# Kernel optimization log

Hardware: AMD Instinct MI355X
Metric: run time of the kernel (lower is better)

Reference implementation:

```python
import jax, jax.numpy as jnp
import numpy as np

D = 1024      # d_model
H = 16        # num_heads
DK = D // H   # head dim
L = 6         # num_layers
DFF = 4 * D   # feed-forward width
V = 32000     # vocab
B = 8         # batch
TP1 = 513     # target tokens (x length); decoded length = 512
S = 1024      # encoder frames
MAXLEN = 512
EPS = 1e-6


def make_pe(max_len, d):
    pos = np.arange(max_len, dtype=np.float64)[:, None]
    i = np.arange(0, d, 2, dtype=np.float64)[None, :]
    ang = pos / np.power(10000.0, i / d)
    pe = np.zeros((max_len, d), dtype=np.float32)
    pe[:, 0::2] = np.sin(ang)
    pe[:, 1::2] = np.cos(ang)
    return jnp.asarray(pe)


def setup_inputs() -> dict:
    key = jax.random.key(0)
    ks = jax.random.split(key, 16)
    sc = 0.02
    inp = {
        'x': jax.random.randint(ks[0], (B, TP1), 0, V, dtype=jnp.int64),
        'encoder_output': jax.random.normal(ks[1], (B, S, D), jnp.float32),
        'emb': jax.random.normal(ks[2], (V, D), jnp.float32) * sc,
        'pe': make_pe(MAXLEN, D),
        # per-layer stacked params; index 0..3 = q,k,v,out projections (in,out layout)
        'attn1_w': jax.random.normal(ks[3], (L, 4, D, D), jnp.float32) * sc,
        'attn1_b': jnp.zeros((L, 4, D), jnp.float32),
        'attn2_w': jax.random.normal(ks[4], (L, 4, D, D), jnp.float32) * sc,
        'attn2_b': jnp.zeros((L, 4, D), jnp.float32),
        'norm_a': jnp.ones((L, 3, D), jnp.float32),
        'norm_b': jnp.zeros((L, 3, D), jnp.float32),
        'ff1_w': jax.random.normal(ks[5], (L, D, DFF), jnp.float32) * sc,
        'ff1_b': jnp.zeros((L, DFF), jnp.float32),
        'ff2_w': jax.random.normal(ks[6], (L, DFF, D), jnp.float32) * sc,
        'ff2_b': jnp.zeros((L, D), jnp.float32),
        'fc_w': jax.random.normal(ks[7], (D, V), jnp.float32) * sc,
        'fc_b': jnp.zeros((V,), jnp.float32),
    }
    return inp


def _norm(x, a, b):
    mu = jnp.mean(x, axis=-1, keepdims=True)
    # torch .std() default is unbiased (ddof=1)
    var = jnp.sum((x - mu) ** 2, axis=-1, keepdims=True) / (x.shape[-1] - 1)
    return a * (x - mu) / (jnp.sqrt(var) + EPS) + b


def _mha(q_in, kv_in, w, b):
    # w: [4, D, D], b: [4, D]; masks in the original are no-ops (bug), omitted.
    bs, tq, _ = q_in.shape
    q = (q_in @ w[0] + b[0]).reshape(bs, tq, H, DK).transpose(0, 2, 1, 3)
    k = (kv_in @ w[1] + b[1]).reshape(bs, -1, H, DK).transpose(0, 2, 1, 3)
    v = (kv_in @ w[2] + b[2]).reshape(bs, -1, H, DK).transpose(0, 2, 1, 3)
    score = jnp.einsum('bhqd,bhkd->bhqk', q, k) / np.sqrt(DK).astype(np.float32)
    attn = jax.nn.softmax(score, axis=-1)
    o = jnp.einsum('bhqk,bhkd->bhqd', attn, v)
    o = o.transpose(0, 2, 1, 3).reshape(bs, tq, D)
    return o @ w[3] + b[3]


def reference(x, encoder_output, emb, pe, attn1_w, attn1_b, attn2_w, attn2_b,
              norm_a, norm_b, ff1_w, ff1_b, ff2_w, ff2_b, fc_w, fc_b):
    t = x.shape[1] - 1
    h = emb[x[:, :-1]] + pe[None, :t, :]  # [B, T, D]
    for l in range(L):
        a1 = _mha(h, h, attn1_w[l], attn1_b[l])
        h = _norm(a1 + h, norm_a[l, 0], norm_b[l, 0])
        a2 = _mha(h, encoder_output, attn2_w[l], attn2_b[l])
        h = _norm(a2 + h, norm_a[l, 1], norm_b[l, 1])
        f = jax.nn.relu(h @ ff1_w[l] + ff1_b[l]) @ ff2_w[l] + ff2_b[l]
        h = _norm(f + h, norm_a[l, 2], norm_b[l, 2])
    logits = h @ fc_w + fc_b  # [B, T, V]
    return jax.nn.log_softmax(logits, axis=-1)
```

## Files before the change

### kernel.cpp

```cpp
#include <hip/hip_runtime.h>

typedef __attribute__((ext_vector_type(4))) float f32x4;
typedef __attribute__((ext_vector_type(8))) __bf16 bfx8;
typedef unsigned short u16;
typedef unsigned int u32;

__device__ __forceinline__ u16 f2bf(float f) {
  u32 u = __builtin_bit_cast(u32, f);
  u = (u + 0x7FFFu + ((u >> 16) & 1u)) >> 16;
  return (u16)u;
}
__device__ __forceinline__ float bf2f(u16 u) {
  return __builtin_bit_cast(float, ((u32)u) << 16);
}

typedef __attribute__((address_space(1))) const void gvoid;
typedef __attribute__((address_space(3))) void svoid;
__device__ __forceinline__ void gload16(const void* g, void* l) {
  __builtin_amdgcn_global_load_lds((gvoid*)g, (svoid*)l, 16, 0, 0);
}

__device__ __forceinline__ float wredsum(float v) {
#pragma unroll
  for (int o = 32; o; o >>= 1) v += __shfl_xor(v, o, 64);
  return v;
}
__device__ __forceinline__ float wredmax(float v) {
#pragma unroll
  for (int o = 32; o; o >>= 1) v = fmaxf(v, __shfl_xor(v, o, 64));
  return v;
}

__global__ __launch_bounds__(256) void wconv_kernel(const float* __restrict__ in,
                                                    u16* __restrict__ out, int K, int N) {
  __shared__ u16 tile[32][33];
  const long z = blockIdx.z;
  const float* iz = in + z * (long)K * N;
  u16* oz = out + z * (long)K * N;
  const int n0 = blockIdx.x << 5, k0 = blockIdx.y << 5;
  const int tx = threadIdx.x & 31, ty = threadIdx.x >> 5;
#pragma unroll
  for (int i = 0; i < 4; ++i)
    tile[ty + 8 * i][tx] = f2bf(iz[(long)(k0 + ty + 8 * i) * N + n0 + tx]);
  __syncthreads();
#pragma unroll
  for (int i = 0; i < 4; ++i)
    oz[(long)(n0 + ty + 8 * i) * K + k0 + tx] = tile[tx][ty + 8 * i];
}

__global__ __launch_bounds__(256) void cvt_kernel(const float* __restrict__ in,
                                                  u16* __restrict__ out, long n) {
  long i = ((long)blockIdx.x * 256 + threadIdx.x) * 4;
  if (i + 3 < n) {
    float4 v = *(const float4*)(in + i);
    ushort4 o = {f2bf(v.x), f2bf(v.y), f2bf(v.z), f2bf(v.w)};
    *(ushort4*)(out + i) = o;
  }
}

__global__ __launch_bounds__(256) void embed_kernel(const int* __restrict__ x,
                                                    const float* __restrict__ emb,
                                                    const float* __restrict__ pe,
                                                    float* __restrict__ h,
                                                    u16* __restrict__ hb) {
  const int row = blockIdx.x;
  const int b = row >> 9, t = row & 511;
  const long tok = (long)x[b * 513 + t];
  const int d = threadIdx.x << 2;
  float4 e = *(const float4*)(emb + tok * 1024 + d);
  float4 p = *(const float4*)(pe + (long)t * 1024 + d);
  float4 v = {e.x + p.x, e.y + p.y, e.z + p.z, e.w + p.w};
  *(float4*)(h + (long)row * 1024 + d) = v;
  ushort4 o = {f2bf(v.x), f2bf(v.y), f2bf(v.z), f2bf(v.w)};
  *(ushort4*)(hb + (long)row * 1024 + d) = o;
}

__global__ __launch_bounds__(256) void addnorm_kernel(const float* __restrict__ delta,
                                                      const float* __restrict__ delta2,
                                                      float* __restrict__ h,
                                                      u16* __restrict__ hb,
                                                      const float* __restrict__ ga,
                                                      const float* __restrict__ gb) {
  __shared__ float r1[4], r2[4];
  const long row = blockIdx.x;
  const int d = threadIdx.x << 2;
  float4 a = *(const float4*)(h + row * 1024 + d);
  float4 q = *(const float4*)(delta + row * 1024 + d);
  float4 q2 = *(const float4*)(delta2 + row * 1024 + d);
  float x0 = a.x + q.x + q2.x, x1 = a.y + q.y + q2.y;
  float x2 = a.z + q.z + q2.z, x3 = a.w + q.w + q2.w;
  float s1 = wredsum(x0 + x1 + x2 + x3);
  float s2 = wredsum(x0 * x0 + x1 * x1 + x2 * x2 + x3 * x3);
  if ((threadIdx.x & 63) == 0) { r1[threadIdx.x >> 6] = s1; r2[threadIdx.x >> 6] = s2; }
  __syncthreads();
  float S1 = r1[0] + r1[1] + r1[2] + r1[3];
  float S2 = r2[0] + r2[1] + r2[2] + r2[3];
  float mu = S1 * (1.0f / 1024.0f);
  float var = (S2 - S1 * mu) * (1.0f / 1023.0f);
  float inv = 1.0f / (sqrtf(fmaxf(var, 0.f)) + 1e-6f);
  float4 g4 = *(const float4*)(ga + d);
  float4 b4 = *(const float4*)(gb + d);
  float y0 = g4.x * (x0 - mu) * inv + b4.x;
  float y1 = g4.y * (x1 - mu) * inv + b4.y;
  float y2 = g4.z * (x2 - mu) * inv + b4.z;
  float y3 = g4.w * (x3 - mu) * inv + b4.w;
  float4 y = {y0, y1, y2, y3};
  *(float4*)(h + row * 1024 + d) = y;
  ushort4 o = {f2bf(y0), f2bf(y1), f2bf(y2), f2bf(y3)};
  *(ushort4*)(hb + row * 1024 + d) = o;
}

__global__ __launch_bounds__(256) void logsoftmax_kernel(float* __restrict__ lg) {
  const long row = blockIdx.x;
  float* lr = lg + row * 32000L;
  float m = -1e30f, s = 0.f;
  for (int j = threadIdx.x; j < 8000; j += 256) {
    float4 v = *(const float4*)(lr + (long)j * 4);
    float lm = fmaxf(fmaxf(v.x, v.y), fmaxf(v.z, v.w));
    if (lm > m) { s *= __expf(m - lm); m = lm; }
    s += __expf(v.x - m) + __expf(v.y - m) + __expf(v.z - m) + __expf(v.w - m);
  }
#pragma unroll
  for (int o = 32; o; o >>= 1) {
    float om = __shfl_xor(m, o, 64), os = __shfl_xor(s, o, 64);
    float M = fmaxf(m, om);
    s = s * __expf(m - M) + os * __expf(om - M);
    m = M;
  }
  __shared__ float rm[4], rs[4];
  if ((threadIdx.x & 63) == 0) { rm[threadIdx.x >> 6] = m; rs[threadIdx.x >> 6] = s; }
  __syncthreads();
  float M = fmaxf(fmaxf(rm[0], rm[1]), fmaxf(rm[2], rm[3]));
  float S = rs[0] * __expf(rm[0] - M) + rs[1] * __expf(rm[1] - M) +
            rs[2] * __expf(rm[2] - M) + rs[3] * __expf(rm[3] - M);
  float lse = M + __logf(S);
  for (int j = threadIdx.x; j < 8000; j += 256) {
    float4 v = *(const float4*)(lr + (long)j * 4);
    v.x -= lse; v.y -= lse; v.z -= lse; v.w -= lse;
    *(float4*)(lr + (long)j * 4) = v;
  }
}

__global__ __launch_bounds__(512) void logsoftmax_bf16_kernel(const u16* __restrict__ lg,
                                                              float* __restrict__ out) {
  __shared__ u16 rl[32000];
  __shared__ float rr[8];
  const long row = blockIdx.x;
  const u16* lr = lg + row * 32000L;
  float* od = out + row * 32000L;
  const int tid = threadIdx.x;
  float m0 = -1e30f, m1 = -1e30f;
  for (int j = tid * 8; j < 32000; j += 4096) {
    ushort4 a = *(const ushort4*)(lr + j);
    ushort4 b = *(const ushort4*)(lr + j + 4);
    *(ushort4*)&rl[j] = a;
    *(ushort4*)&rl[j + 4] = b;
    m0 = fmaxf(m0, fmaxf(fmaxf(bf2f(a.x), bf2f(a.y)), fmaxf(bf2f(a.z), bf2f(a.w))));
    m1 = fmaxf(m1, fmaxf(fmaxf(bf2f(b.x), bf2f(b.y)), fmaxf(bf2f(b.z), bf2f(b.w))));
  }
  float m = wredmax(fmaxf(m0, m1));
  if ((tid & 63) == 0) rr[tid >> 6] = m;
  __syncthreads();
  m = fmaxf(fmaxf(fmaxf(rr[0], rr[1]), fmaxf(rr[2], rr[3])),
            fmaxf(fmaxf(rr[4], rr[5]), fmaxf(rr[6], rr[7])));
  __syncthreads();
  float s0 = 0.f, s1 = 0.f;
  for (int j = tid * 8; j < 32000; j += 4096) {
    ushort4 a = *(const ushort4*)&rl[j];
    ushort4 b = *(const ushort4*)&rl[j + 4];
    s0 += __expf(bf2f(a.x) - m) + __expf(bf2f(a.y) - m) +
          __expf(bf2f(a.z) - m) + __expf(bf2f(a.w) - m);
    s1 += __expf(bf2f(b.x) - m) + __expf(bf2f(b.y) - m) +
          __expf(bf2f(b.z) - m) + __expf(bf2f(b.w) - m);
  }
  float s = wredsum(s0 + s1);
  if ((tid & 63) == 0) rr[tid >> 6] = s;
  __syncthreads();
  s = rr[0] + rr[1] + rr[2] + rr[3] + rr[4] + rr[5] + rr[6] + rr[7];
  const float lse = m + __logf(s);
  for (int j = tid * 8; j < 32000; j += 4096) {
    ushort4 a = *(const ushort4*)&rl[j];
    ushort4 b = *(const ushort4*)&rl[j + 4];
    float4 o0 = {bf2f(a.x) - lse, bf2f(a.y) - lse, bf2f(a.z) - lse, bf2f(a.w) - lse};
    float4 o1 = {bf2f(b.x) - lse, bf2f(b.y) - lse, bf2f(b.z) - lse, bf2f(b.w) - lse};
    *(float4*)(od + j) = o0;
    *(float4*)(od + j + 4) = o1;
  }
}

template <int SKV>
__global__ __launch_bounds__(256) void attn_kernel(const u16* __restrict__ Q,
                                                   const u16* __restrict__ Kb,
                                                   const u16* __restrict__ Vt,
                                                   u16* __restrict__ ctx) {
  __shared__ u16 Kl[4096];
  __shared__ u16 Vl[4096];
  __shared__ u16 Pl[4][16][72];
  const int tid = threadIdx.x, lane = tid & 63, wave = tid >> 6;
  const int l15 = lane & 15, lg = lane >> 4;
  const int bh = blockIdx.y;
  const int qrow = blockIdx.x * 64 + wave * 16 + l15;
  const u16* qp = Q + ((long)bh * 512 + qrow) * 64 + lg * 8;
  bfx8 qf0 = *(const bfx8*)(qp);
  bfx8 qf1 = *(const bfx8*)(qp + 32);

  const int srow = tid >> 3;
  const int schunk = (tid & 7) ^ (srow & 7);
  const u16* Kbb = Kb + ((long)bh * SKV + srow) * 64 + schunk * 8;
  const u16* Vtb2 = Vt + ((long)bh * 64 + srow) * SKV + schunk * 8;

  const f32x4 zf = {0.f, 0.f, 0.f, 0.f};
  f32x4 acc_o[4] = {zf, zf, zf, zf};
  float mrun = -1e30f, lrun = 0.f;
  const int swk = l15 & 7;

#pragma unroll 1
  for (int kv0 = 0; kv0 < SKV; kv0 += 64) {
    gload16(Kbb + (long)kv0 * 64, &Kl[tid * 8]);
    gload16(Kbb + (long)(kv0 + 32) * 64, &Kl[2048 + tid * 8]);
    gload16(Vtb2 + kv0, &Vl[tid * 8]);
    gload16(Vtb2 + (long)32 * SKV + kv0, &Vl[2048 + tid * 8]);
    __syncthreads();
    f32x4 sacc[4];
#pragma unroll
    for (int kvt = 0; kvt < 4; ++kvt) {
      const int krow = kvt * 16 + l15;
      bfx8 kf0 = *(const bfx8*)&Kl[krow * 64 + ((lg ^ swk) << 3)];
      bfx8 kf1 = *(const bfx8*)&Kl[krow * 64 + (((4 + lg) ^ swk) << 3)];
      f32x4 t = __builtin_amdgcn_mfma_f32_16x16x32_bf16(kf0, qf0, zf, 0, 0, 0);
      sacc[kvt] = __builtin_amdgcn_mfma_f32_16x16x32_bf16(kf1, qf1, t, 0, 0, 0);
    }
    float pm = -1e30f;
#pragma unroll
    for (int kvt = 0; kvt < 4; ++kvt)
#pragma unroll
      for (int r = 0; r < 4; ++r) pm = fmaxf(pm, sacc[kvt][r]);
    pm = fmaxf(pm, __shfl_xor(pm, 16, 64));
    pm = fmaxf(pm, __shfl_xor(pm, 32, 64));
    pm *= 0.125f;
    const float mnew = fmaxf(mrun, pm);
    const float corr = __expf(mrun - mnew);
    float psum = 0.f;
#pragma unroll
    for (int kvt = 0; kvt < 4; ++kvt)
#pragma unroll
      for (int r = 0; r < 4; ++r) {
        float p = __expf(sacc[kvt][r] * 0.125f - mnew);
        psum += p;
        Pl[wave][l15][kvt * 16 + lg * 4 + r] = f2bf(p);
      }
    psum += __shfl_xor(psum, 16, 64);
    psum += __shfl_xor(psum, 32, 64);
    lrun = lrun * corr + psum;
    mrun = mnew;
#pragma unroll
    for (int dt = 0; dt < 4; ++dt) {
      acc_o[dt][0] *= corr; acc_o[dt][1] *= corr;
      acc_o[dt][2] *= corr; acc_o[dt][3] *= corr;
    }
    bfx8 pf0 = *(const bfx8*)&Pl[wave][l15][lg * 8];
    bfx8 pf1 = *(const bfx8*)&Pl[wave][l15][32 + lg * 8];
#pragma unroll
    for (int dt = 0; dt < 4; ++dt) {
      const int vrow = dt * 16 + l15;
      bfx8 vf0 = *(const bfx8*)&Vl[vrow * 64 + ((lg ^ swk) << 3)];
      bfx8 vf1 = *(const bfx8*)&Vl[vrow * 64 + (((4 + lg) ^ swk) << 3)];
      acc_o[dt] = __builtin_amdgcn_mfma_f32_16x16x32_bf16(vf0, pf0, acc_o[dt], 0, 0, 0);
      acc_o[dt] = __builtin_amdgcn_mfma_f32_16x16x32_bf16(vf1, pf1, acc_o[dt], 0, 0, 0);
    }
    __syncthreads();
  }
  const float inv = 1.0f / lrun;
  const int b = bh >> 4, hh = bh & 15;
  u16* crow = ctx + ((long)b * 512 + qrow) * 1024 + hh * 64;
#pragma unroll
  for (int dt = 0; dt < 4; ++dt)
#pragma unroll
    for (int r = 0; r < 4; ++r)
      crow[dt * 16 + lg * 4 + r] = f2bf(acc_o[dt][r] * inv);
}

template <int BM, int BN, int WMW, int WNW, int EPI, bool RELU>
__global__ __launch_bounds__(256) void gemm_bt(const u16* __restrict__ A, long sAz, int lda,
                                               const u16* __restrict__ Bt, long sBz, int ldb,
                                               const float* __restrict__ bias,
                                               void* __restrict__ out, long sCz, int ldc,
                                               int K, int Ttok) {
  constexpr int WROWS = BM / WMW, WCOLS = BN / WNW;
  constexpr int MI = WROWS / 16, NI = WCOLS / 16;
  __shared__ u16 As[BM * 32];
  __shared__ u16 Bs[BN * 32];
  const int tid = threadIdx.x, lane = tid & 63, wave = tid >> 6;
  const int l15 = lane & 15, lg = lane >> 4;
  const int wm = wave / WNW, wn = wave % WNW;
  const int bx = blockIdx.x, by = blockIdx.y;
  const long z = blockIdx.z;
  const int srow = tid >> 2, scol = (tid & 3) << 3;
  const u16* Aa = A + z * sAz + (long)(by * BM + srow) * lda + scol;
  const u16* Ba = Bt + z * sBz + (long)(bx * BN + srow) * ldb + scol;

  f32x4 acc[MI][NI];
#pragma unroll
  for (int i = 0; i < MI; ++i)
#pragma unroll
    for (int j = 0; j < NI; ++j) acc[i][j] = (f32x4){0.f, 0.f, 0.f, 0.f};

  for (int kt = 0; kt < K; kt += 32) {
#pragma unroll
    for (int i = 0; i < BM / 64; ++i)
      gload16(Aa + (long)i * 64 * lda + kt, &As[i * 2048 + tid * 8]);
#pragma unroll
    for (int i = 0; i < BN / 64; ++i)
      gload16(Ba + (long)i * 64 * ldb + kt, &Bs[i * 2048 + tid * 8]);
    __syncthreads();
    bfx8 afr[MI], bfr[NI];
#pragma unroll
    for (int i = 0; i < MI; ++i)
      afr[i] = *(const bfx8*)&As[(wm * WROWS + i * 16 + l15) * 32 + (lg << 3)];
#pragma unroll
    for (int j = 0; j < NI; ++j)
      bfr[j] = *(const bfx8*)&Bs[(wn * WCOLS + j * 16 + l15) * 32 + (lg << 3)];
#pragma unroll
    for (int i = 0; i < MI; ++i)
#pragma unroll
      for (int j = 0; j < NI; ++j)
        acc[i][j] = __builtin_amdgcn_mfma_f32_16x16x32_bf16(afr[i], bfr[j], acc[i][j], 0, 0, 0);
    __syncthreads();
  }

  const int gm0 = by * BM + wm * WROWS;
  const int gn0 = bx * BN + wn * WCOLS;
#pragma unroll
  for (int i = 0; i < MI; ++i) {
#pragma unroll
    for (int j = 0; j < NI; ++j) {
      const int gn = gn0 + j * 16 + l15;
      const float bv = (bias && z == 0) ? bias[gn] : 0.f;
#pragma unroll
      for (int r = 0; r < 4; ++r) {
        const int gm = gm0 + i * 16 + (lg << 2) + r;
        float v = acc[i][j][r] + bv;
        if (RELU) v = fmaxf(v, 0.f);
        if constexpr (EPI == 0) {
          ((float*)out)[z * sCz + (long)gm * ldc + gn] = v;
        } else if constexpr (EPI == 1) {
          ((u16*)out)[z * sCz + (long)gm * ldc + gn] = f2bf(v);
        } else if constexpr (EPI == 3) {
          const int b = gm / Ttok, t = gm - b * Ttok;
          const int hh = gn >> 6, dk = gn & 63;
          ((u16*)out)[(((long)(b * 16 + hh) * Ttok + t) << 6) + dk] = f2bf(v);
        }
      }
    }
  }
}

#define MMAQ(hm, hn)                                                                   \
  {                                                                                    \
    _Pragma("unroll") for (int kk = 0; kk < 2; ++kk)                                   \
        _Pragma("unroll") for (int i = 0; i < 4; ++i)                                  \
            _Pragma("unroll") for (int jn = 0; jn < 2; ++jn)                           \
                acc[(hm)*4 + i][(hn)*2 + jn] = __builtin_amdgcn_mfma_f32_16x16x32_bf16( \
                    a[i][kk], b[jn][kk], acc[(hm)*4 + i][(hn)*2 + jn], 0, 0, 0);       \
  }

template <int EPI, bool RELU>
__global__ __launch_bounds__(512, 2) void gemm256(const u16* __restrict__ A, int lda,
                                                  const u16* __restrict__ Bt, int ldb,
                                                  const float* __restrict__ bias,
                                                  void* __restrict__ out, int ldc, int K,
                                                  int Ttok, void* __restrict__ out2,
                                                  void* __restrict__ out3, int gx) {
  __shared__ u16 lds[2][2][2][8192];
  const int tid = threadIdx.x, lane = tid & 63;
  const int wid = tid >> 6, wm = wid >> 2, wn = wid & 3;
  const int l15 = lane & 15, lg = lane >> 4;
  const int S = gx >> 3;
  const int xcd = blockIdx.x & 7, idx = blockIdx.x >> 3;
  const int mt = xcd * S + idx % S;
  const int nt_ = idx / S;
  const int NT = K >> 6;

  const int r0 = tid >> 3;
  const int blkx = (tid & 7) ^ (r0 & 7);
  const u16* Abase = A + (long)(mt * 256 + r0) * lda + blkx * 8;
  const u16* Bbase = Bt + (long)(nt_ * 256 + r0) * ldb + blkx * 8;

  auto stageA = [&](int s, int half) {
    const int kts = (s < NT ? s : NT - 1) << 6;
    const u16* g = Abase + (long)(half * 128) * lda + kts;
    gload16(g, &lds[s & 1][0][half][tid * 8]);
    gload16(g + (long)64 * lda, &lds[s & 1][0][half][(512 + tid) * 8]);
  };
  auto stageB = [&](int s, int half) {
    const int kts = (s < NT ? s : NT - 1) << 6;
    const u16* g = Bbase + (long)(half * 128) * ldb + kts;
    gload16(g, &lds[s & 1][1][half][tid * 8]);
    gload16(g + (long)64 * ldb, &lds[s & 1][1][half][(512 + tid) * 8]);
  };

  f32x4 acc[8][4];
#pragma unroll
  for (int i = 0; i < 8; ++i)
#pragma unroll
    for (int j = 0; j < 4; ++j) acc[i][j] = (f32x4){0.f, 0.f, 0.f, 0.f};
  bfx8 a[4][2], b[2][2];

  const int sw = l15 & 7;
  auto loadA = [&](int buf, int hm) {
#pragma unroll
    for (int i = 0; i < 4; ++i) {
      const int row = hm * 64 + i * 16 + l15;
#pragma unroll
      for (int kk = 0; kk < 2; ++kk)
        a[i][kk] = *(const bfx8*)&lds[buf][0][wm][row * 64 + (((kk * 4 + lg) ^ sw) << 3)];
    }
  };
  auto loadB = [&](int buf, int hn) {
#pragma unroll
    for (int jn = 0; jn < 2; ++jn) {
      const int row = (wn & 1) * 64 + hn * 32 + jn * 16 + l15;
#pragma unroll
      for (int kk = 0; kk < 2; ++kk)
        b[jn][kk] = *(const bfx8*)&lds[buf][1][wn >> 1][row * 64 + (((kk * 4 + lg) ^ sw) << 3)];
    }
  };

  stageA(0, 0); stageA(0, 1); stageB(0, 0); stageB(0, 1);
  stageA(1, 0); stageA(1, 1);
  asm volatile("s_waitcnt vmcnt(4)" ::: "memory");
  __builtin_amdgcn_s_barrier();

  for (int t = 0; t < NT; ++t) {
    const int p = t & 1;
    loadA(p, 0); loadB(p, 0);
    stageB(t + 1, 0);
    __builtin_amdgcn_s_barrier();
    asm volatile("s_waitcnt lgkmcnt(0)" ::: "memory");
    __builtin_amdgcn_s_setprio(1);
    MMAQ(0, 0);
    __builtin_amdgcn_s_setprio(0);
    __builtin_amdgcn_s_barrier();
    loadB(p, 1);
    stageB(t + 1, 1);
    __builtin_amdgcn_s_barrier();
    asm volatile("s_waitcnt lgkmcnt(0)" ::: "memory");
    __builtin_amdgcn_s_setprio(1);
    MMAQ(0, 1);
    __builtin_amdgcn_s_setprio(0);
    __builtin_amdgcn_s_barrier();
    loadA(p, 1); loadB(p, 0);
    stageA(t + 2, 0);
    __builtin_amdgcn_s_barrier();
    asm volatile("s_waitcnt lgkmcnt(0)" ::: "memory");
    __builtin_amdgcn_s_setprio(1);
    MMAQ(1, 0);
    __builtin_amdgcn_s_setprio(0);
    __builtin_amdgcn_s_barrier();
    loadB(p, 1);
    stageA(t + 2, 1);
    asm volatile("s_waitcnt vmcnt(4)" ::: "memory");
    __builtin_amdgcn_s_barrier();
    asm volatile("s_waitcnt lgkmcnt(0)" ::: "memory");
    __builtin_amdgcn_s_setprio(1);
    MMAQ(1, 1);
    __builtin_amdgcn_s_setprio(0);
    __builtin_amdgcn_s_barrier();
  }

  const int gm0 = mt * 256 + wm * 128;
  const int gn0 = nt_ * 256 + wn * 64;
#pragma unroll
  for (int ii = 0; ii < 8; ++ii) {
#pragma unroll
    for (int jj = 0; jj < 4; ++jj) {
      const int gn = gn0 + jj * 16 + l15;
      const float bv = bias ? bias[gn] : 0.f;
#pragma unroll
      for (int r = 0; r < 4; ++r) {
        const int gm = gm0 + ii * 16 + (lg << 2) + r;
        float v = acc[ii][jj][r] + bv;
        if (RELU) v = fmaxf(v, 0.f);
        if constexpr (EPI == 0) {
          ((float*)out)[(long)gm * ldc + gn] = v;
        } else if constexpr (EPI == 1) {
          ((u16*)out)[(long)gm * ldc + gn] = f2bf(v);
        } else if constexpr (EPI == 6) {
          const int bq = gm / Ttok, t2 = gm - bq * Ttok;
          const int sec = gn >> 10, w1 = gn & 1023;
          const int hh = w1 >> 6, dk = w1 & 63;
          const u16 val = f2bf(v);
          if (sec == 0)
            ((u16*)out)[(((long)(bq * 16 + hh) * Ttok + t2) << 6) + dk] = val;
          else if (sec == 1)
            ((u16*)out2)[(((long)(bq * 16 + hh) * Ttok + t2) << 6) + dk] = val;
          else
            ((u16*)out3)[((long)((bq * 16 + hh) << 6) + dk) * Ttok + t2] = val;
        } else if constexpr (EPI == 7) {
          const int bq = gm / Ttok, t2 = gm - bq * Ttok;
          const int sec = gn >> 10, w1 = gn & 1023;
          const int hh = w1 >> 6, dk = w1 & 63;
          const u16 val = f2bf(v);
          if (sec == 0)
            ((u16*)out)[(((long)(bq * 16 + hh) * Ttok + t2) << 6) + dk] = val;
          else
            ((u16*)out2)[((long)((bq * 16 + hh) << 6) + dk) * Ttok + t2] = val;
        }
      }
    }
  }
}

extern "C" void kernel_launch(void* const* d_in, const int* in_sizes, int n_in,
                              void* d_out, int out_size, void* d_ws, size_t ws_size,
                              hipStream_t stream) {
  const int* x = (const int*)d_in[0];
  const float* enc = (const float*)d_in[1];
  const float* emb = (const float*)d_in[2];
  const float* pe = (const float*)d_in[3];
  const float* a1w = (const float*)d_in[4];
  const float* a1b = (const float*)d_in[5];
  const float* a2w = (const float*)d_in[6];
  const float* a2b = (const float*)d_in[7];
  const float* nra = (const float*)d_in[8];
  const float* nrb = (const float*)d_in[9];
  const float* f1w = (const float*)d_in[10];
  const float* f1b = (const float*)d_in[11];
  const float* f2w = (const float*)d_in[12];
  const float* f2b = (const float*)d_in[13];
  const float* fcw = (const float*)d_in[14];
  const float* fcb = (const float*)d_in[15];
  float* out = (float*)d_out;

  char* base = (char*)d_ws;
  size_t off = 0;
  auto alloc = [&](size_t bytes) -> void* {
    void* p = base + off;
    off += (bytes + 255) & ~(size_t)255;
    return p;
  };
  const long wsz = 1024 * 1024;
  const bool big = ws_size >= (600ull << 20);
  u16* wT = (u16*)alloc(96ull * wsz * 2);
  u16* encb = (u16*)alloc(8ull * wsz * 2);
  float* h = (float*)alloc(4ull * wsz * 4);
  u16* hb = (u16*)alloc(4ull * wsz * 2);
  u16* qb = (u16*)alloc(4ull * wsz * 2);
  u16* kb = (u16*)alloc(8ull * wsz * 2);
  u16* vtb = (u16*)alloc(8ull * wsz * 2);
  u16* ctxb = (u16*)alloc(4ull * wsz * 2);
  float* af = (float*)alloc(4ull * wsz * 4);
  float* af2 = (float*)alloc(4ull * wsz * 4);
  u16* midb = (u16*)alloc(16ull * wsz * 2);
  u16* fcT = qb;
  u16* lgb = big ? (u16*)alloc(4096ull * 32000 * 2) : nullptr;

  u16* wTa1 = wT;
  u16* wTa2 = wT + 24 * wsz;
  u16* wTf1 = wT + 48 * wsz;
  u16* wTf2 = wT + 72 * wsz;

  cvt_kernel<<<dim3(8192), dim3(256), 0, stream>>>(enc, encb, 8ll * wsz);
  embed_kernel<<<dim3(4096), dim3(256), 0, stream>>>(x, emb, pe, h, hb);
  wconv_kernel<<<dim3(32, 32, 24), dim3(256), 0, stream>>>(a1w, wTa1, 1024, 1024);
  wconv_kernel<<<dim3(32, 32, 24), dim3(256), 0, stream>>>(a2w, wTa2, 1024, 1024);
  wconv_kernel<<<dim3(128, 32, 6), dim3(256), 0, stream>>>(f1w, wTf1, 1024, 4096);
  wconv_kernel<<<dim3(32, 128, 6), dim3(256), 0, stream>>>(f2w, wTf2, 4096, 1024);

  for (int l = 0; l < 6; ++l) {
    const float* b1 = a1b + (long)l * 4096;
    const float* b2 = a2b + (long)l * 4096;
    const u16* w1 = wTa1 + (long)l * 4 * wsz;
    const u16* w2 = wTa2 + (long)l * 4 * wsz;

    gemm256<6, false><<<dim3(192), dim3(512), 0, stream>>>(
        hb, 1024, w1, 1024, b1, qb, 0, 1024, 512, kb, vtb, 16);
    attn_kernel<512><<<dim3(8, 128), dim3(256), 0, stream>>>(qb, kb, vtb, ctxb);
    gemm_bt<128, 128, 2, 2, 0, false><<<dim3(8, 32, 2), dim3(256), 0, stream>>>(
        ctxb, 512, 1024, w1 + 3 * wsz, 512, 1024, b1 + 3072, af, 4194304, 1024, 512, 0);
    addnorm_kernel<<<dim3(4096), dim3(256), 0, stream>>>(
        af, af2, h, hb, nra + (l * 3 + 0) * 1024, nrb + (l * 3 + 0) * 1024);

    gemm_bt<128, 128, 2, 2, 3, false><<<dim3(8, 32, 1), dim3(256), 0, stream>>>(
        hb, 0, 1024, w2, 0, 1024, b2, qb, 0, 0, 1024, 512);
    gemm256<7, false><<<dim3(256), dim3(512), 0, stream>>>(
        encb, 1024, w2 + wsz, 1024, b2 + 1024, kb, 0, 1024, 1024, vtb, nullptr, 32);
    attn_kernel<1024><<<dim3(8, 128), dim3(256), 0, stream>>>(qb, kb, vtb, ctxb);
    gemm_bt<128, 128, 2, 2, 0, false><<<dim3(8, 32, 2), dim3(256), 0, stream>>>(
        ctxb, 512, 1024, w2 + 3 * wsz, 512, 1024, b2 + 3072, af, 4194304, 1024, 512, 0);
    addnorm_kernel<<<dim3(4096), dim3(256), 0, stream>>>(
        af, af2, h, hb, nra + (l * 3 + 1) * 1024, nrb + (l * 3 + 1) * 1024);

    gemm256<1, true><<<dim3(256), dim3(512), 0, stream>>>(
        hb, 1024, wTf1 + (long)l * 4 * wsz, 1024, f1b + (long)l * 4096, midb, 4096, 1024, 0,
        nullptr, nullptr, 16);
    gemm_bt<128, 128, 2, 2, 0, false><<<dim3(8, 32, 2), dim3(256), 0, stream>>>(
        midb, 2048, 4096, wTf2 + (long)l * 4 * wsz, 2048, 4096, f2b + (long)l * 1024, af,
        4194304, 1024, 2048, 0);
    addnorm_kernel<<<dim3(4096), dim3(256), 0, stream>>>(
        af, af2, h, hb, nra + (l * 3 + 2) * 1024, nrb + (l * 3 + 2) * 1024);
  }

  wconv_kernel<<<dim3(1000, 32, 1), dim3(256), 0, stream>>>(fcw, fcT, 1024, 32000);
  if (big) {
    gemm256<1, false><<<dim3(2000), dim3(512), 0, stream>>>(
        hb, 1024, fcT, 1024, fcb, lgb, 32000, 1024, 0, nullptr, nullptr, 16);
    logsoftmax_bf16_kernel<<<dim3(4096), dim3(512), 0, stream>>>(lgb, out);
  } else {
    gemm256<0, false><<<dim3(2000), dim3(512), 0, stream>>>(
        hb, 1024, fcT, 1024, fcb, out, 32000, 1024, 0, nullptr, nullptr, 16);
    logsoftmax_kernel<<<dim3(4096), dim3(256), 0, stream>>>(out);
  }
}
```

Measured before the change: 3.211 ms.

## Load attention K/V directly from global, lazily rescale softmax, simplify GEMM tile mapping

```diff
diff --git a/kernel.cpp b/kernel.cpp
--- a/kernel.cpp
+++ b/kernel.cpp
@@ -193,8 +193,6 @@
                                                    const u16* __restrict__ Kb,
                                                    const u16* __restrict__ Vt,
                                                    u16* __restrict__ ctx) {
-  __shared__ u16 Kl[4096];
-  __shared__ u16 Vl[4096];
   __shared__ u16 Pl[4][16][72];
   const int tid = threadIdx.x, lane = tid & 63, wave = tid >> 6;
   const int l15 = lane & 15, lg = lane >> 4;
@@ -203,30 +201,21 @@
   const u16* qp = Q + ((long)bh * 512 + qrow) * 64 + lg * 8;
   bfx8 qf0 = *(const bfx8*)(qp);
   bfx8 qf1 = *(const bfx8*)(qp + 32);
-
-  const int srow = tid >> 3;
-  const int schunk = (tid & 7) ^ (srow & 7);
-  const u16* Kbb = Kb + ((long)bh * SKV + srow) * 64 + schunk * 8;
-  const u16* Vtb2 = Vt + ((long)bh * 64 + srow) * SKV + schunk * 8;
+  const u16* Kbh = Kb + (long)bh * SKV * 64;
+  const u16* Vbh = Vt + (long)bh * 64 * SKV;
 
   const f32x4 zf = {0.f, 0.f, 0.f, 0.f};
   f32x4 acc_o[4] = {zf, zf, zf, zf};
   float mrun = -1e30f, lrun = 0.f;
-  const int swk = l15 & 7;
 
 #pragma unroll 1
   for (int kv0 = 0; kv0 < SKV; kv0 += 64) {
-    gload16(Kbb + (long)kv0 * 64, &Kl[tid * 8]);
-    gload16(Kbb + (long)(kv0 + 32) * 64, &Kl[2048 + tid * 8]);
-    gload16(Vtb2 + kv0, &Vl[tid * 8]);
-    gload16(Vtb2 + (long)32 * SKV + kv0, &Vl[2048 + tid * 8]);
-    __syncthreads();
     f32x4 sacc[4];
 #pragma unroll
     for (int kvt = 0; kvt < 4; ++kvt) {
-      const int krow = kvt * 16 + l15;
-      bfx8 kf0 = *(const bfx8*)&Kl[krow * 64 + ((lg ^ swk) << 3)];
-      bfx8 kf1 = *(const bfx8*)&Kl[krow * 64 + (((4 + lg) ^ swk) << 3)];
+      const u16* kr = Kbh + (long)(kv0 + kvt * 16 + l15) * 64 + lg * 8;
+      bfx8 kf0 = *(const bfx8*)kr;
+      bfx8 kf1 = *(const bfx8*)(kr + 32);
       f32x4 t = __builtin_amdgcn_mfma_f32_16x16x32_bf16(kf0, qf0, zf, 0, 0, 0);
       sacc[kvt] = __builtin_amdgcn_mfma_f32_16x16x32_bf16(kf1, qf1, t, 0, 0, 0);
     }
@@ -238,8 +227,8 @@
     pm = fmaxf(pm, __shfl_xor(pm, 16, 64));
     pm = fmaxf(pm, __shfl_xor(pm, 32, 64));
     pm *= 0.125f;
-    const float mnew = fmaxf(mrun, pm);
-    const float corr = __expf(mrun - mnew);
+    const bool grow = !__all(pm <= mrun);
+    const float mnew = grow ? fmaxf(mrun, pm) : mrun;
     float psum = 0.f;
 #pragma unroll
     for (int kvt = 0; kvt < 4; ++kvt)
@@ -251,24 +240,28 @@
       }
     psum += __shfl_xor(psum, 16, 64);
     psum += __shfl_xor(psum, 32, 64);
-    lrun = lrun * corr + psum;
-    mrun = mnew;
-#pragma unroll
-    for (int dt = 0; dt < 4; ++dt) {
-      acc_o[dt][0] *= corr; acc_o[dt][1] *= corr;
-      acc_o[dt][2] *= corr; acc_o[dt][3] *= corr;
+    if (grow) {
+      const float corr = __expf(mrun - mnew);
+      lrun = lrun * corr + psum;
+      mrun = mnew;
+#pragma unroll
+      for (int dt = 0; dt < 4; ++dt) {
+        acc_o[dt][0] *= corr; acc_o[dt][1] *= corr;
+        acc_o[dt][2] *= corr; acc_o[dt][3] *= corr;
+      }
+    } else {
+      lrun += psum;
     }
     bfx8 pf0 = *(const bfx8*)&Pl[wave][l15][lg * 8];
     bfx8 pf1 = *(const bfx8*)&Pl[wave][l15][32 + lg * 8];
 #pragma unroll
     for (int dt = 0; dt < 4; ++dt) {
-      const int vrow = dt * 16 + l15;
-      bfx8 vf0 = *(const bfx8*)&Vl[vrow * 64 + ((lg ^ swk) << 3)];
-      bfx8 vf1 = *(const bfx8*)&Vl[vrow * 64 + (((4 + lg) ^ swk) << 3)];
+      const u16* vr = Vbh + (long)(dt * 16 + l15) * SKV + kv0 + lg * 8;
+      bfx8 vf0 = *(const bfx8*)vr;
+      bfx8 vf1 = *(const bfx8*)(vr + 32);
       acc_o[dt] = __builtin_amdgcn_mfma_f32_16x16x32_bf16(vf0, pf0, acc_o[dt], 0, 0, 0);
       acc_o[dt] = __builtin_amdgcn_mfma_f32_16x16x32_bf16(vf1, pf1, acc_o[dt], 0, 0, 0);
     }
-    __syncthreads();
   }
   const float inv = 1.0f / lrun;
   const int b = bh >> 4, hh = bh & 15;
@@ -375,10 +368,8 @@
   const int tid = threadIdx.x, lane = tid & 63;
   const int wid = tid >> 6, wm = wid >> 2, wn = wid & 3;
   const int l15 = lane & 15, lg = lane >> 4;
-  const int S = gx >> 3;
-  const int xcd = blockIdx.x & 7, idx = blockIdx.x >> 3;
-  const int mt = xcd * S + idx % S;
-  const int nt_ = idx / S;
+  const int mt = blockIdx.x % gx;
+  const int nt_ = blockIdx.x / gx;
   const int NT = K >> 6;
 
   const int r0 = tid >> 3;
```

After: 3.860 ms. 20.2% more time.
